# Kernel tuning notes

Hardware: AMD Instinct MI355X
Metric: run time of the kernel (lower is better)

Reference implementation:

```python
import jax, jax.numpy as jnp
import numpy as np


def setup_inputs() -> dict:
    key = jax.random.key(0)
    k1, k2 = jax.random.split(key)
    B, DIM, T, SIZE = 64, 512, 2048, 1024
    H = jax.random.normal(k1, (B, DIM, T), dtype=jnp.float32)
    units = jax.random.normal(k2, (DIM, SIZE), dtype=jnp.float32)
    return {"H": H, "units": units}


def reference(H, units):
    # H: (B, dim, T), units: (dim, size)
    # Original: C[b, s, t] = exp(-||H[b,:,t] - units[:,s]||^2) normalized over s.
    # exp(-d^2) / sum_s exp(-d^2) == softmax(-d^2, axis=s).
    Ht = jnp.swapaxes(H, 1, 2)                      # (B, T, dim)
    h_sq = jnp.sum(Ht * Ht, axis=-1, keepdims=True)  # (B, T, 1)
    m_sq = jnp.sum(units * units, axis=0)            # (size,)
    cross = jnp.einsum('btd,ds->bts', Ht, units)     # (B, T, size) GEMM
    sqdist = h_sq - 2.0 * cross + m_sq               # (B, T, size)
    C = jax.nn.softmax(-sqdist, axis=-1)             # normalize over codebook
    return jnp.swapaxes(C, 1, 2)                     # (B, size, T)
```

## Files before the change

### kernel.cpp

```cpp
#include <hip/hip_runtime.h>
#include <stdint.h>


typedef unsigned short u16;
typedef __attribute__((ext_vector_type(8))) short short8;
typedef __attribute__((ext_vector_type(4))) float f32x4;
typedef __attribute__((ext_vector_type(16))) float f32x16;

#define B_DIM 64
#define DIM   512
#define T_DIM 2048
#define S_DIM 1024

#define B_LO_O 65536
#define REDM_O 131072
#define REDS_O 135168
#define SM_SZ  139264

__device__ __forceinline__ u16 f32_to_bf16(float f) {
  uint32_t u = __float_as_uint(f);
  uint32_t r = u + 0x7FFFu + ((u >> 16) & 1u);
  return (u16)(r >> 16);
}
__device__ __forceinline__ float bf16_to_f32(u16 h) {
  return __uint_as_float(((uint32_t)h) << 16);
}

__global__ __launch_bounds__(256) void k_prep_units(const float* __restrict__ units,
                                                    u16* __restrict__ UpH, u16* __restrict__ UpL,
                                                    float* __restrict__ msq) {
  const int s0 = blockIdx.x * 4;
  const int tid = threadIdx.x;
  const int lane = tid & 63, wv = tid >> 6;
  float acc0 = 0.f, acc1 = 0.f, acc2 = 0.f, acc3 = 0.f;
#pragma unroll
  for (int j = 0; j < 2; ++j) {
    const int d = tid + j * 256;
    const float4 v = *(const float4*)(units + (size_t)d * S_DIM + s0);
    acc0 += v.x * v.x; acc1 += v.y * v.y; acc2 += v.z * v.z; acc3 += v.w * v.w;
    const int dbase = (d >> 4) * 16384 + ((d >> 3) & 1) * 256 + (d & 7);
    const float fv[4] = {v.x, v.y, v.z, v.w};
#pragma unroll
    for (int q = 0; q < 4; ++q) {
      const int s = s0 + q;
      const int idx = dbase + ((s >> 5) * 64 + (s & 31)) * 8;
      const u16 h = f32_to_bf16(fv[q]);
      UpH[idx] = h;
      UpL[idx] = f32_to_bf16(fv[q] - bf16_to_f32(h));
    }
  }
#pragma unroll
  for (int off = 1; off < 64; off <<= 1) {
    acc0 += __shfl_xor(acc0, off);
    acc1 += __shfl_xor(acc1, off);
    acc2 += __shfl_xor(acc2, off);
    acc3 += __shfl_xor(acc3, off);
  }
  __shared__ float part[4][4];
  if (lane == 0) { part[wv][0] = acc0; part[wv][1] = acc1; part[wv][2] = acc2; part[wv][3] = acc3; }
  __syncthreads();
  if (tid < 4) msq[s0 + tid] = part[0][tid] + part[1][tid] + part[2][tid] + part[3][tid];
}

__global__ __launch_bounds__(256) void k_prep_h(const float* __restrict__ H,
                                                u16* __restrict__ BpH, u16* __restrict__ BpL) {
  __shared__ float tile[64 * 68];
  const int bx = blockIdx.x;
  const int d0 = blockIdx.y * 64;
  const int b = blockIdx.z;
  const int t0 = bx * 64;
  const int tid = threadIdx.x;
#pragma unroll
  for (int j = 0; j < 4; ++j) {
    const int chunk = tid + j * 256;
    const int r = chunk >> 4, c4 = (chunk & 15) * 4;
    const float4 v = *(const float4*)(H + ((size_t)(b * DIM + d0 + r)) * T_DIM + t0 + c4);
    *(float4*)(&tile[r * 68 + c4]) = v;
  }
  __syncthreads();
#pragma unroll
  for (int j = 0; j < 2; ++j) {
    const int chunk = tid + j * 256;
    const int q = chunk >> 3, e8 = (chunk & 7) * 8;
    union { u16 us[8]; uint4 v4; } hi, lo;
#pragma unroll
    for (int k = 0; k < 8; ++k) {
      const float f = tile[(e8 + k) * 68 + q];
      const u16 h = f32_to_bf16(f);
      hi.us[k] = h;
      lo.us[k] = f32_to_bf16(f - bf16_to_f32(h));
    }
    const int dg = d0 + e8;
    const int chunkB = (q >> 5) * 64 + ((dg >> 3) & 1) * 32 + (q & 31);
    const size_t o = ((((size_t)b * 32 + bx) * 32 + (dg >> 4)) * 128 + chunkB) * 8;
    *(uint4*)(BpH + o) = hi.v4;
    *(uint4*)(BpL + o) = lo.v4;
  }
}

__device__ __forceinline__ void gl16(const void* g, void* l) {
  __builtin_amdgcn_global_load_lds((const __attribute__((address_space(1))) void*)g,
                                   (__attribute__((address_space(3))) void*)l, 16, 0, 0);
}

#define WAITV0() asm volatile("s_waitcnt vmcnt(0)" ::: "memory")
#define SYNCPT() do { __builtin_amdgcn_s_barrier(); __builtin_amdgcn_sched_barrier(0); } while (0)

__global__ __launch_bounds__(1024, 4) void k_fused(const u16* __restrict__ UpH, const u16* __restrict__ UpL,
                                                   const u16* __restrict__ BpH, const u16* __restrict__ BpL,
                                                   const float* __restrict__ msq,
                                                   float* __restrict__ out) {
  __shared__ __align__(16) char sm[SM_SZ];
  const int tid = threadIdx.x;
  const int lane = tid & 63, wv = tid >> 6;
  const int l31 = lane & 31, lhi = lane >> 5;
  const int sw = wv;

  const int tgx = blockIdx.x;
  const int t00 = tgx * 64;
  const int bb = blockIdx.y;

  const char* const aH = (const char*)UpH + sw * 2048 + lane * 16;
  const char* const aL = (const char*)UpL + sw * 2048 + lane * 16;
  const size_t bgBase = (size_t)(bb * 32 + tgx) * 65536;
  const char* const pBH = (const char*)BpH + bgBase;
  const char* const pBL = (const char*)BpL + bgBase;

#pragma unroll
  for (int r = 0; r < 4; ++r) {
    const int off = (tid + r * 1024) * 16;
    gl16(pBH + off, sm + off);
  }
#pragma unroll
  for (int r = 0; r < 4; ++r) {
    const int off = (tid + r * 1024) * 16;
    gl16(pBL + off, sm + B_LO_O + off);
  }

  f32x16 acc[2][2];
#pragma unroll
  for (int mt = 0; mt < 2; ++mt)
#pragma unroll
    for (int nt = 0; nt < 2; ++nt)
#pragma unroll
      for (int r = 0; r < 16; ++r)
        acc[mt][nt][r] = 0.f;

  WAITV0();
  SYNCPT();

#pragma unroll 1
  for (int ks = 0; ks < 32; ++ks) {
    const int bo = ks * 2048 + lane * 16;
    short8 bh0 = *(const short8*)(sm + bo);
    short8 bh1 = *(const short8*)(sm + bo + 1024);
    short8 bl0 = *(const short8*)(sm + B_LO_O + bo);
    short8 bl1 = *(const short8*)(sm + B_LO_O + bo + 1024);
    const size_t ko = (size_t)ks << 15;
    short8 ah0 = *(const short8*)(aH + ko);
    short8 ah1 = *(const short8*)(aH + ko + 1024);
    short8 al0 = *(const short8*)(aL + ko);
    short8 al1 = *(const short8*)(aL + ko + 1024);
    __builtin_amdgcn_s_setprio(1);
    acc[0][0] = __builtin_amdgcn_mfma_f32_32x32x16_bf16(ah0, bh0, acc[0][0], 0, 0, 0);
    acc[0][1] = __builtin_amdgcn_mfma_f32_32x32x16_bf16(ah0, bh1, acc[0][1], 0, 0, 0);
    acc[1][0] = __builtin_amdgcn_mfma_f32_32x32x16_bf16(ah1, bh0, acc[1][0], 0, 0, 0);
    acc[1][1] = __builtin_amdgcn_mfma_f32_32x32x16_bf16(ah1, bh1, acc[1][1], 0, 0, 0);
    acc[0][0] = __builtin_amdgcn_mfma_f32_32x32x16_bf16(ah0, bl0, acc[0][0], 0, 0, 0);
    acc[0][1] = __builtin_amdgcn_mfma_f32_32x32x16_bf16(ah0, bl1, acc[0][1], 0, 0, 0);
    acc[1][0] = __builtin_amdgcn_mfma_f32_32x32x16_bf16(ah1, bl0, acc[1][0], 0, 0, 0);
    acc[1][1] = __builtin_amdgcn_mfma_f32_32x32x16_bf16(ah1, bl1, acc[1][1], 0, 0, 0);
    acc[0][0] = __builtin_amdgcn_mfma_f32_32x32x16_bf16(al0, bh0, acc[0][0], 0, 0, 0);
    acc[0][1] = __builtin_amdgcn_mfma_f32_32x32x16_bf16(al0, bh1, acc[0][1], 0, 0, 0);
    acc[1][0] = __builtin_amdgcn_mfma_f32_32x32x16_bf16(al1, bh0, acc[1][0], 0, 0, 0);
    acc[1][1] = __builtin_amdgcn_mfma_f32_32x32x16_bf16(al1, bh1, acc[1][1], 0, 0, 0);
    __builtin_amdgcn_s_setprio(0);
  }

  float* redM = (float*)(sm + REDM_O);
  float* redS = (float*)(sm + REDS_O);
  float mx0 = -3.0e38f, mx1 = -3.0e38f;
#pragma unroll
  for (int mt = 0; mt < 2; ++mt) {
    const int sb = sw * 64 + mt * 32 + lhi * 4;
#pragma unroll
    for (int q = 0; q < 4; ++q) {
      const f32x4 mq = *(const f32x4*)(msq + sb + q * 8);
#pragma unroll
      for (int r = 0; r < 4; ++r) {
        const int reg = q * 4 + r;
        const float v0 = 2.f * acc[mt][0][reg] - mq[r];
        const float v1 = 2.f * acc[mt][1][reg] - mq[r];
        acc[mt][0][reg] = v0; acc[mt][1][reg] = v1;
        mx0 = fmaxf(mx0, v0); mx1 = fmaxf(mx1, v1);
      }
    }
  }
  mx0 = fmaxf(mx0, __shfl_xor(mx0, 32));
  mx1 = fmaxf(mx1, __shfl_xor(mx1, 32));
  if (lane < 32) { redM[wv * 64 + l31] = mx0; redM[wv * 64 + 32 + l31] = mx1; }
  __syncthreads();
  float M0 = redM[l31], M1 = redM[32 + l31];
#pragma unroll
  for (int w = 1; w < 16; ++w) {
    M0 = fmaxf(M0, redM[w * 64 + l31]);
    M1 = fmaxf(M1, redM[w * 64 + 32 + l31]);
  }
  float s0 = 0.f, s1 = 0.f;
#pragma unroll
  for (int mt = 0; mt < 2; ++mt)
#pragma unroll
    for (int reg = 0; reg < 16; ++reg) {
      const float e0 = __expf(acc[mt][0][reg] - M0);
      const float e1 = __expf(acc[mt][1][reg] - M1);
      acc[mt][0][reg] = e0; acc[mt][1][reg] = e1;
      s0 += e0; s1 += e1;
    }
  s0 += __shfl_xor(s0, 32);
  s1 += __shfl_xor(s1, 32);
  if (lane < 32) { redS[wv * 64 + l31] = s0; redS[wv * 64 + 32 + l31] = s1; }
  __syncthreads();
  float S0 = redS[l31], S1 = redS[32 + l31];
#pragma unroll
  for (int w = 1; w < 16; ++w) {
    S0 += redS[w * 64 + l31];
    S1 += redS[w * 64 + 32 + l31];
  }
  const float r0 = 1.0f / S0, r1 = 1.0f / S1;

  float* const outb = out + ((size_t)bb << 21);
  const int tc0 = t00 + l31, tc1 = t00 + 32 + l31;
#pragma unroll
  for (int mt = 0; mt < 2; ++mt) {
    const int sb = sw * 64 + mt * 32 + lhi * 4;
#pragma unroll
    for (int q = 0; q < 4; ++q)
#pragma unroll
      for (int r = 0; r < 4; ++r) {
        const int srow = sb + q * 8 + r;
        const int reg = q * 4 + r;
        outb[(size_t)srow * T_DIM + tc0] = acc[mt][0][reg] * r0;
        outb[(size_t)srow * T_DIM + tc1] = acc[mt][1][reg] * r1;
      }
  }
}

extern "C" void kernel_launch(void* const* d_in, const int* in_sizes, int n_in,
                              void* d_out, int out_size, void* d_ws, size_t ws_size,
                              hipStream_t stream) {
  (void)in_sizes; (void)n_in; (void)out_size; (void)ws_size;
  const float* H = (const float*)d_in[0];
  const float* units = (const float*)d_in[1];
  float* out = (float*)d_out;
  char* ws = (char*)d_ws;
  u16* BpH = (u16*)(ws);
  u16* BpL = (u16*)(ws + 134217728);
  u16* UpH = (u16*)(ws + 268435456);
  u16* UpL = (u16*)(ws + 269484032);
  float* msq = (float*)(ws + 270532608);

  k_prep_units<<<dim3(S_DIM / 4), 256, 0, stream>>>(units, UpH, UpL, msq);
  k_prep_h<<<dim3(T_DIM / 64, DIM / 64, B_DIM), 256, 0, stream>>>(H, BpH, BpL);
  k_fused<<<dim3(T_DIM / 64, B_DIM), 1024, 0, stream>>>(UpH, UpL, BpH, BpL, msq, out);
}
```

Measured before the change: 597.0 us.

## Double-buffer A and B k-slices in LDS with async global-to-LDS prefetch

Replaces the one-time full load of the B tile into LDS, and the per-iteration direct global reads of the units (A) fragments, with a two-slot LDS ring. Each k-step's A hi/lo and B hi/lo slices are loaded with global_load_lds two steps ahead, so loads overlap with the MFMA work. The aim is to hide the global latency of the A reads that previously stalled each iteration. In exchange it adds a vmcnt wait and a workgroup barrier every iteration, and slightly more LDS.

```diff
diff --git a/kernel.cpp b/kernel.cpp
--- a/kernel.cpp
+++ b/kernel.cpp
@@ -12,10 +12,13 @@
 #define T_DIM 2048
 #define S_DIM 1024
 
-#define B_LO_O 65536
-#define REDM_O 131072
-#define REDS_O 135168
-#define SM_SZ  139264
+#define SLOT    69632
+#define A_LO    32768
+#define B_HI_O  65536
+#define B_LO_O2 67584
+#define REDM_O  139264
+#define REDS_O  143360
+#define SM_SZ   147456
 
 __device__ __forceinline__ u16 f32_to_bf16(float f) {
   uint32_t u = __float_as_uint(f);
@@ -114,28 +117,34 @@
   const int tid = threadIdx.x;
   const int lane = tid & 63, wv = tid >> 6;
   const int l31 = lane & 31, lhi = lane >> 5;
+  const int lane16 = lane * 16;
   const int sw = wv;
 
   const int tgx = blockIdx.x;
   const int t00 = tgx * 64;
   const int bb = blockIdx.y;
 
-  const char* const aH = (const char*)UpH + sw * 2048 + lane * 16;
-  const char* const aL = (const char*)UpL + sw * 2048 + lane * 16;
+  const char* const pAh = (const char*)UpH;
+  const char* const pAl = (const char*)UpL;
   const size_t bgBase = (size_t)(bb * 32 + tgx) * 65536;
-  const char* const pBH = (const char*)BpH + bgBase;
-  const char* const pBL = (const char*)BpL + bgBase;
-
-#pragma unroll
-  for (int r = 0; r < 4; ++r) {
-    const int off = (tid + r * 1024) * 16;
-    gl16(pBH + off, sm + off);
-  }
-#pragma unroll
-  for (int r = 0; r < 4; ++r) {
-    const int off = (tid + r * 1024) * 16;
-    gl16(pBL + off, sm + B_LO_O + off);
-  }
+  const char* const pBh = (const char*)BpH + bgBase;
+  const char* const pBl = (const char*)BpL + bgBase;
+
+#define STAGE(KS, SLOTB) do {                                                 \
+    const size_t koA = (size_t)(KS) << 15;                                    \
+    const int d0_ = (2 * wv) * 1024 + lane16;                                 \
+    const int d1_ = d0_ + 1024;                                               \
+    gl16(pAh + koA + d0_, sm + (SLOTB) + d0_);                                \
+    gl16(pAh + koA + d1_, sm + (SLOTB) + d1_);                                \
+    gl16(pAl + koA + d0_, sm + (SLOTB) + A_LO + d0_);                         \
+    gl16(pAl + koA + d1_, sm + (SLOTB) + A_LO + d1_);                         \
+    if (wv < 4) {                                                             \
+      const char* src_ = (wv < 2) ? pBh : pBl;                                \
+      const int reg_ = (wv < 2) ? B_HI_O : B_LO_O2;                           \
+      const int bo_ = (wv & 1) * 1024 + lane16;                               \
+      gl16(src_ + (size_t)(KS) * 2048 + bo_, sm + (SLOTB) + reg_ + bo_);      \
+    }                                                                         \
+  } while (0)
 
   f32x16 acc[2][2];
 #pragma unroll
@@ -146,21 +155,23 @@
       for (int r = 0; r < 16; ++r)
         acc[mt][nt][r] = 0.f;
 
+  STAGE(0, 0);
+  STAGE(1, SLOT);
   WAITV0();
   SYNCPT();
 
 #pragma unroll 1
-  for (int ks = 0; ks < 32; ++ks) {
-    const int bo = ks * 2048 + lane * 16;
-    short8 bh0 = *(const short8*)(sm + bo);
-    short8 bh1 = *(const short8*)(sm + bo + 1024);
-    short8 bl0 = *(const short8*)(sm + B_LO_O + bo);
-    short8 bl1 = *(const short8*)(sm + B_LO_O + bo + 1024);
-    const size_t ko = (size_t)ks << 15;
-    short8 ah0 = *(const short8*)(aH + ko);
-    short8 ah1 = *(const short8*)(aH + ko + 1024);
-    short8 al0 = *(const short8*)(aL + ko);
-    short8 al1 = *(const short8*)(aL + ko + 1024);
+  for (int k = 0; k < 32; ++k) {
+    const char* sl = sm + (k & 1) * SLOT;
+    const int a0 = (2 * wv) * 1024 + lane16;
+    short8 ah0 = *(const short8*)(sl + a0);
+    short8 ah1 = *(const short8*)(sl + a0 + 1024);
+    short8 al0 = *(const short8*)(sl + A_LO + a0);
+    short8 al1 = *(const short8*)(sl + A_LO + a0 + 1024);
+    short8 bh0 = *(const short8*)(sl + B_HI_O + lane16);
+    short8 bh1 = *(const short8*)(sl + B_HI_O + 1024 + lane16);
+    short8 bl0 = *(const short8*)(sl + B_LO_O2 + lane16);
+    short8 bl1 = *(const short8*)(sl + B_LO_O2 + 1024 + lane16);
     __builtin_amdgcn_s_setprio(1);
     acc[0][0] = __builtin_amdgcn_mfma_f32_32x32x16_bf16(ah0, bh0, acc[0][0], 0, 0, 0);
     acc[0][1] = __builtin_amdgcn_mfma_f32_32x32x16_bf16(ah0, bh1, acc[0][1], 0, 0, 0);
@@ -175,6 +186,9 @@
     acc[1][0] = __builtin_amdgcn_mfma_f32_32x32x16_bf16(al1, bh0, acc[1][0], 0, 0, 0);
     acc[1][1] = __builtin_amdgcn_mfma_f32_32x32x16_bf16(al1, bh1, acc[1][1], 0, 0, 0);
     __builtin_amdgcn_s_setprio(0);
+    WAITV0();
+    SYNCPT();
+    if (k + 2 < 32) STAGE(k + 2, (k & 1) * SLOT);
   }
 
   float* redM = (float*)(sm + REDM_O);
```

New measurement: 576.1 us. 1.04x faster.
